# Kernel tuning notes

Hardware: AMD Instinct MI355X
Metric: run time of the kernel (lower is better)

Reference implementation:

```python
import jax, jax.numpy as jnp
import numpy as np

D = 1024
HS = 64
NH = D // HS
NEG_INF = -1e30


def setup_inputs() -> dict:
    key = jax.random.key(0)
    ks = jax.random.split(key, 8)
    B, S = 4, 2048
    x = jax.random.normal(ks[0], (B, S, D), dtype=jnp.float32)
    y = jax.random.normal(ks[1], (B, S, D), dtype=jnp.float32)
    pad_mask = jnp.ones((B, S), dtype=jnp.int32)
    time_attention = jnp.ones((S, S), dtype=jnp.int32)
    scale = 1.0 / np.sqrt(D)
    Wq = jax.random.normal(ks[2], (D, D), dtype=jnp.float32) * scale
    Wk = jax.random.normal(ks[3], (D, D), dtype=jnp.float32) * scale
    Wv = jax.random.normal(ks[4], (D, D), dtype=jnp.float32) * scale
    Wp = jax.random.normal(ks[5], (D, D), dtype=jnp.float32) * scale
    bp = jnp.zeros((D,), dtype=jnp.float32)
    return {"x": x, "y": y, "pad_mask": pad_mask, "time_attention": time_attention,
            "Wq": Wq, "Wk": Wk, "Wv": Wv, "Wp": Wp, "bp": bp}


def reference(x, y, pad_mask, time_attention, Wq, Wk, Wv, Wp, bp):
    B, S, _ = x.shape
    Sy = y.shape[1]
    # q/k/v projections (Linear: x @ W.T), split into heads -> [B, H, S, hs]
    q = (y @ Wq.T).reshape(B, Sy, NH, HS).transpose(0, 2, 1, 3)
    k = (x @ Wk.T).reshape(B, S, NH, HS).transpose(0, 2, 1, 3)
    v = (x @ Wv.T).reshape(B, S, NH, HS).transpose(0, 2, 1, 3)
    # scaled scores [B, H, Sy, S]
    att = jnp.einsum('bhqe,bhke->bhqk', q, k) * (HS ** -0.5)
    # causal mask (tril[:S, :S])
    causal = jnp.tril(jnp.ones((S, S), dtype=jnp.bool_))
    att = jnp.where(causal[None, None, :Sy, :], att, NEG_INF)
    # pad mask over kv positions
    att = jnp.where(pad_mask[:, None, None, :] != 0, att, NEG_INF)
    # time attention mask [Sq, Sk]
    att = jnp.where(time_attention[None, None, :Sy, :] != 0, att, NEG_INF)
    p = jax.nn.softmax(att, axis=-1)  # dropout p=0 -> identity
    out = jnp.einsum('bhqk,bhke->bhqe', p, v)
    out = out.transpose(0, 2, 1, 3).reshape(B, Sy, D)
    return out @ Wp.T + bp
```

## Files before the change

### kernel.cpp

```cpp
#include <hip/hip_runtime.h>
#include <hip/hip_bf16.h>
#include <stdint.h>
#include <stddef.h>


typedef __attribute__((ext_vector_type(4))) float f32x4;
typedef __attribute__((ext_vector_type(8))) short s16x8;
typedef __attribute__((ext_vector_type(4))) float float4v;
typedef __attribute__((ext_vector_type(4))) int i32x4;
typedef __attribute__((ext_vector_type(2))) unsigned int u32x2;

#define DEV __device__ __forceinline__

constexpr int Bsz = 4, Sseq = 2048, Dm = 1024, NHn = 16, HSn = 64;
constexpr float QSCALE = 0.125f * 1.4426950408889634f;

constexpr size_t SZ_BF_XY = (size_t)Bsz * Sseq * Dm * 2;
constexpr size_t SZ_W     = (size_t)Dm * Dm * 2;
constexpr size_t OFF_XBF  = 0;
constexpr size_t OFF_YBF  = OFF_XBF + SZ_BF_XY;
constexpr size_t OFF_WQ   = OFF_YBF + SZ_BF_XY;
constexpr size_t OFF_WK   = OFF_WQ + SZ_W;
constexpr size_t OFF_WV   = OFF_WK + SZ_W;
constexpr size_t OFF_WP   = OFF_WV + SZ_W;
constexpr size_t OFF_QWS  = OFF_WP + SZ_W;
constexpr size_t OFF_KWS  = OFF_QWS + SZ_BF_XY;
constexpr size_t OFF_VTWS = OFF_KWS + SZ_BF_XY;
constexpr size_t OFF_OWS  = OFF_VTWS + SZ_BF_XY;
constexpr size_t OFF_FLAG = OFF_OWS + SZ_BF_XY;

DEV unsigned short f2bf(float f) {
  union { float f; unsigned int u; } v; v.f = f;
  unsigned int r = (v.u + 0x7FFFu + ((v.u >> 16) & 1u)) >> 16;
  return (unsigned short)r;
}

DEV void gll16(const void* g, void* l) {
  __builtin_amdgcn_global_load_lds((const __attribute__((address_space(1))) unsigned int*)g,
                                   (__attribute__((address_space(3))) unsigned int*)l, 16, 0, 0);
}

DEV unsigned int cvtpk(float a, float b) {
  unsigned int r;
  asm("v_cvt_pk_bf16_f32 %0, %1, %2" : "=v"(r) : "v"(a), "v"(b));
  return r;
}

__global__ void cvt_all(const float* __restrict__ x, const float* __restrict__ y,
                        const float* __restrict__ Wq, const float* __restrict__ Wk,
                        const float* __restrict__ Wv, const float* __restrict__ Wp,
                        const int* __restrict__ pad, const int* __restrict__ tmask,
                        char* __restrict__ ws, int* __restrict__ flags) {
  const int blk = blockIdx.x;
  if (blk >= 10240) {
    int bad = 0;
    if (blk < 10248) {
      const i32x4 v = ((const i32x4*)pad)[(blk - 10240) * 256 + threadIdx.x];
      bad = (v[0] == 0) | (v[1] == 0) | (v[2] == 0) | (v[3] == 0);
    } else {
      const i32x4* tp = (const i32x4*)tmask + ((size_t)(blk - 10248) * 256 + threadIdx.x) * 2;
      i32x4 v0 = tp[0], v1 = tp[1];
      bad = (v0[0] == 0) | (v0[1] == 0) | (v0[2] == 0) | (v0[3] == 0) |
            (v1[0] == 0) | (v1[1] == 0) | (v1[2] == 0) | (v1[3] == 0);
    }
    if (__builtin_amdgcn_ballot_w64(bad) != 0 && (threadIdx.x & 63) == 0)
      atomicOr(flags, 1);
    return;
  }
  const float* src;
  unsigned short* dst;
  int b8;
  float scale = 1.f;
  if (blk < 4096)      { src = x;  dst = (unsigned short*)(ws + OFF_XBF); b8 = blk; }
  else if (blk < 8192) { src = y;  dst = (unsigned short*)(ws + OFF_YBF); b8 = blk - 4096; }
  else if (blk < 8704) { src = Wq; dst = (unsigned short*)(ws + OFF_WQ);  b8 = blk - 8192; scale = QSCALE; }
  else if (blk < 9216) { src = Wk; dst = (unsigned short*)(ws + OFF_WK);  b8 = blk - 8704; }
  else if (blk < 9728) { src = Wv; dst = (unsigned short*)(ws + OFF_WV);  b8 = blk - 9216; }
  else                 { src = Wp; dst = (unsigned short*)(ws + OFF_WP);  b8 = blk - 9728; }
  const size_t i = (size_t)b8 * 256 + threadIdx.x;
  const float4v* s = (const float4v*)src + i * 2;
  float4v a = s[0], b = s[1];
  s16x8 o;
  o[0] = (short)f2bf(a[0] * scale); o[1] = (short)f2bf(a[1] * scale);
  o[2] = (short)f2bf(a[2] * scale); o[3] = (short)f2bf(a[3] * scale);
  o[4] = (short)f2bf(b[0] * scale); o[5] = (short)f2bf(b[1] * scale);
  o[6] = (short)f2bf(b[2] * scale); o[7] = (short)f2bf(b[3] * scale);
  *(s16x8*)(dst + i * 8) = o;
}

__global__ __launch_bounds__(256) void q_gemm(const unsigned short* __restrict__ A,
                                              const unsigned short* __restrict__ W,
                                              unsigned short* __restrict__ outb) {
  constexpr int K = 1024;
  __shared__ unsigned short sm[8192];
  unsigned short* lA = sm;
  unsigned short* lB = sm + 4096;
  const int tid = threadIdx.x;
  const int w = tid >> 6, lane = tid & 63, lo = lane & 15, hi = lane >> 4;
  const int wm = w >> 1, wn = w & 1;
  const int m0 = blockIdx.x * 128, n0 = blockIdx.y * 128;
  f32x4 acc[4][4] = {};

  for (int k0 = 0; k0 < K; k0 += 32) {
#pragma unroll
    for (int h = 0; h < 2; ++h) {
      int c = w * 64 + h * 256 + lane;
      gll16(A + (size_t)(m0 + (c >> 2)) * K + k0 + (c & 3) * 8, lA + (size_t)(w * 64 + h * 256) * 8);
      gll16(W + (size_t)(n0 + (c >> 2)) * K + k0 + (c & 3) * 8, lB + (size_t)(w * 64 + h * 256) * 8);
    }
    __syncthreads();
    s16x8 af[4], bfr[4];
#pragma unroll
    for (int mi = 0; mi < 4; ++mi) af[mi] = *(const s16x8*)&lA[(wm * 64 + mi * 16 + lo) * 32 + hi * 8];
#pragma unroll
    for (int ni = 0; ni < 4; ++ni) bfr[ni] = *(const s16x8*)&lB[(wn * 64 + ni * 16 + lo) * 32 + hi * 8];
#pragma unroll
    for (int mi = 0; mi < 4; ++mi)
#pragma unroll
      for (int ni = 0; ni < 4; ++ni)
        acc[mi][ni] = __builtin_amdgcn_mfma_f32_16x16x32_bf16(af[mi], bfr[ni], acc[mi][ni], 0, 0, 0);
    __syncthreads();
  }
#pragma unroll
  for (int mi = 0; mi < 4; ++mi)
#pragma unroll
    for (int ni = 0; ni < 4; ++ni)
#pragma unroll
      for (int j = 0; j < 4; ++j) {
        int m = m0 + wm * 64 + mi * 16 + hi * 4 + j;
        int n = n0 + wn * 64 + ni * 16 + lo;
        int b = m >> 11, s = m & 2047, hh = n >> 6, e = n & 63;
        outb[((size_t)(b * NHn + hh) * Sseq + s) * HSn + e] = f2bf(acc[mi][ni][j]);
      }
}

__global__ __launch_bounds__(256, 2) void kv_gemm(const unsigned short* __restrict__ A,
                                                  const unsigned short* __restrict__ Wk,
                                                  const unsigned short* __restrict__ Wv,
                                                  unsigned short* __restrict__ kws,
                                                  unsigned short* __restrict__ vtw) {
  constexpr int K = 1024;
  __shared__ unsigned short sm[17408];
  unsigned short* lA = sm;
  unsigned short* lBk = sm + 4096;
  unsigned short* lBv = sm + 8192;
  const int tid = threadIdx.x;
  const int w = tid >> 6, lane = tid & 63, lo = lane & 15, hi = lane >> 4;
  const int wm = w >> 1, wn = w & 1;
  const int m0 = blockIdx.x * 128, n0 = blockIdx.y * 128;
  f32x4 acck[4][4] = {}, accv[4][4] = {};

  for (int k0 = 0; k0 < K; k0 += 32) {
#pragma unroll
    for (int h = 0; h < 2; ++h) {
      int c = w * 64 + h * 256 + lane;
      size_t roff = (size_t)(c >> 2) * K + k0 + (c & 3) * 8;
      size_t loff = (size_t)(w * 64 + h * 256) * 8;
      gll16(A + (size_t)m0 * K + roff, lA + loff);
      gll16(Wk + (size_t)n0 * K + roff, lBk + loff);
      gll16(Wv + (size_t)n0 * K + roff, lBv + loff);
    }
    __syncthreads();
    s16x8 af[4], bfk[4], bfv[4];
#pragma unroll
    for (int mi = 0; mi < 4; ++mi) af[mi] = *(const s16x8*)&lA[(wm * 64 + mi * 16 + lo) * 32 + hi * 8];
#pragma unroll
    for (int ni = 0; ni < 4; ++ni) {
      bfk[ni] = *(const s16x8*)&lBk[(wn * 64 + ni * 16 + lo) * 32 + hi * 8];
      bfv[ni] = *(const s16x8*)&lBv[(wn * 64 + ni * 16 + lo) * 32 + hi * 8];
    }
#pragma unroll
    for (int mi = 0; mi < 4; ++mi)
#pragma unroll
      for (int ni = 0; ni < 4; ++ni) {
        acck[mi][ni] = __builtin_amdgcn_mfma_f32_16x16x32_bf16(af[mi], bfk[ni], acck[mi][ni], 0, 0, 0);
        accv[mi][ni] = __builtin_amdgcn_mfma_f32_16x16x32_bf16(af[mi], bfv[ni], accv[mi][ni], 0, 0, 0);
      }
    __syncthreads();
  }

#pragma unroll
  for (int mi = 0; mi < 4; ++mi)
#pragma unroll
    for (int ni = 0; ni < 4; ++ni)
#pragma unroll
      for (int j = 0; j < 4; ++j) {
        int m = m0 + wm * 64 + mi * 16 + hi * 4 + j;
        int n = n0 + wn * 64 + ni * 16 + lo;
        int b = m >> 11, s = m & 2047, hh = n >> 6, e = n & 63;
        kws[((size_t)(b * NHn + hh) * Sseq + s) * HSn + e] = f2bf(acck[mi][ni][j]);
      }
  __syncthreads();
#pragma unroll
  for (int mi = 0; mi < 4; ++mi)
#pragma unroll
    for (int ni = 0; ni < 4; ++ni)
#pragma unroll
      for (int j = 0; j < 4; ++j) {
        int ml = wm * 64 + mi * 16 + hi * 4 + j;
        int nl = wn * 64 + ni * 16 + lo;
        sm[(size_t)nl * 136 + ml] = f2bf(accv[mi][ni][j]);
      }
  __syncthreads();
  int nl = tid >> 1, half = tid & 1;
  int b = m0 >> 11, hh = (n0 + nl) >> 6, e = (n0 + nl) & 63;
  unsigned short* dst = vtw + ((size_t)(b * NHn + hh) * HSn + e) * Sseq + (m0 & 2047) + half * 64;
#pragma unroll
  for (int i = 0; i < 8; ++i)
    *(s16x8*)(dst + i * 8) = *(const s16x8*)&sm[(size_t)nl * 136 + half * 64 + i * 8];
}

__global__ __launch_bounds__(256) void gemm_p(const unsigned short* __restrict__ A,
                                              const unsigned short* __restrict__ W,
                                              float* __restrict__ outf,
                                              const float* __restrict__ bias) {
  constexpr int K = 1024;
  __shared__ unsigned short sm[8192];
  unsigned short* lA = sm;
  unsigned short* lB = sm + 4096;
  const int tid = threadIdx.x;
  const int w = tid >> 6, lane = tid & 63, lo = lane & 15, hi = lane >> 4;
  const int wm = w >> 1, wn = w & 1;
  const int m0 = blockIdx.x * 128, n0 = blockIdx.y * 128;
  f32x4 acc[4][4] = {};
  for (int k0 = 0; k0 < K; k0 += 32) {
#pragma unroll
    for (int h = 0; h < 2; ++h) {
      int c = w * 64 + h * 256 + lane;
      gll16(A + (size_t)(m0 + (c >> 2)) * K + k0 + (c & 3) * 8, lA + (size_t)(w * 64 + h * 256) * 8);
      gll16(W + (size_t)(n0 + (c >> 2)) * K + k0 + (c & 3) * 8, lB + (size_t)(w * 64 + h * 256) * 8);
    }
    __syncthreads();
    s16x8 af[4], bfr[4];
#pragma unroll
    for (int mi = 0; mi < 4; ++mi) af[mi] = *(const s16x8*)&lA[(wm * 64 + mi * 16 + lo) * 32 + hi * 8];
#pragma unroll
    for (int ni = 0; ni < 4; ++ni) bfr[ni] = *(const s16x8*)&lB[(wn * 64 + ni * 16 + lo) * 32 + hi * 8];
#pragma unroll
    for (int mi = 0; mi < 4; ++mi)
#pragma unroll
      for (int ni = 0; ni < 4; ++ni)
        acc[mi][ni] = __builtin_amdgcn_mfma_f32_16x16x32_bf16(af[mi], bfr[ni], acc[mi][ni], 0, 0, 0);
    __syncthreads();
  }
  float bv[4];
#pragma unroll
  for (int ni = 0; ni < 4; ++ni) bv[ni] = bias[n0 + wn * 64 + ni * 16 + lo];
#pragma unroll
  for (int mi = 0; mi < 4; ++mi)
#pragma unroll
    for (int ni = 0; ni < 4; ++ni)
#pragma unroll
      for (int j = 0; j < 4; ++j) {
        int m = m0 + wm * 64 + mi * 16 + hi * 4 + j;
        int n = n0 + wn * 64 + ni * 16 + lo;
        outf[(size_t)m * 1024 + n] = acc[mi][ni][j] + bv[ni];
      }
}

DEV void attn_unit16(const unsigned short* __restrict__ kbc,
                     const unsigned short* __restrict__ vbc,
                     const s16x8 (&qf)[2], f32x4 (&oacc)[4],
                     float& mrun, float& lrun,
                     unsigned short* __restrict__ pbw,
                     int k0, int qw0, int lo, int hi, int b,
                     const int* __restrict__ pad, const int* __restrict__ tmask,
                     bool trivial) {
  if (k0 > qw0 + 15) return;

  f32x4 st[4];
#pragma unroll
  for (int t = 0; t < 4; ++t) {
    f32x4 z = {0.f, 0.f, 0.f, 0.f};
#pragma unroll
    for (int kk = 0; kk < 2; ++kk) {
      s16x8 kfr = *(const s16x8*)&kbc[(t * 16 + lo) * 72 + kk * 32 + hi * 8];
      z = __builtin_amdgcn_mfma_f32_16x16x32_bf16(kfr, qf[kk], z, 0, 0, 0);
    }
    st[t] = z;
  }
  const int qg = qw0 + lo;
  if (k0 + 63 > qw0) {
#pragma unroll
    for (int t = 0; t < 4; ++t)
#pragma unroll
      for (int j = 0; j < 4; ++j)
        if (k0 + t * 16 + hi * 4 + j > qg) st[t][j] = -3e38f;
  }
  if (!trivial) {
#pragma unroll
    for (int t = 0; t < 4; ++t)
#pragma unroll
      for (int j = 0; j < 4; ++j) {
        int kg = k0 + t * 16 + hi * 4 + j;
        if (!pad[b * Sseq + kg] || !tmask[(size_t)qg * Sseq + kg]) st[t][j] = -3e38f;
      }
  }
  float m0v = fmaxf(fmaxf(st[0][0], st[0][1]), fmaxf(st[0][2], st[0][3]));
  float m1v = fmaxf(fmaxf(st[1][0], st[1][1]), fmaxf(st[1][2], st[1][3]));
  float m2v = fmaxf(fmaxf(st[2][0], st[2][1]), fmaxf(st[2][2], st[2][3]));
  float m3v = fmaxf(fmaxf(st[3][0], st[3][1]), fmaxf(st[3][2], st[3][3]));
  float mx = fmaxf(fmaxf(m0v, m1v), fmaxf(m2v, m3v));
  mx = fmaxf(mx, __shfl_xor(mx, 16, 64));
  mx = fmaxf(mx, __shfl_xor(mx, 32, 64));
  const float mnew = fmaxf(mrun, mx);
  const float al = __builtin_amdgcn_exp2f(mrun - mnew);
  mrun = mnew;
  float r0 = 0.f, r1 = 0.f, r2 = 0.f, r3 = 0.f;
#pragma unroll
  for (int j = 0; j < 4; ++j) {
    float p0 = __builtin_amdgcn_exp2f(st[0][j] - mnew); st[0][j] = p0; r0 += p0;
    float p1 = __builtin_amdgcn_exp2f(st[1][j] - mnew); st[1][j] = p1; r1 += p1;
    float p2 = __builtin_amdgcn_exp2f(st[2][j] - mnew); st[2][j] = p2; r2 += p2;
    float p3 = __builtin_amdgcn_exp2f(st[3][j] - mnew); st[3][j] = p3; r3 += p3;
  }
  float rs = (r0 + r1) + (r2 + r3);
  rs += __shfl_xor(rs, 16, 64);
  rs += __shfl_xor(rs, 32, 64);
  lrun = lrun * al + rs;
#pragma unroll
  for (int et = 0; et < 4; ++et) oacc[et] *= al;
#pragma unroll
  for (int t = 0; t < 4; ++t) {
    u32x2 dd = {cvtpk(st[t][0], st[t][1]), cvtpk(st[t][2], st[t][3])};
    *(u32x2*)&pbw[lo * 72 + t * 16 + hi * 4] = dd;
  }
  s16x8 pf[2];
#pragma unroll
  for (int kk = 0; kk < 2; ++kk)
    pf[kk] = *(const s16x8*)&pbw[lo * 72 + kk * 32 + hi * 8];
#pragma unroll
  for (int et = 0; et < 4; ++et)
#pragma unroll
    for (int kk = 0; kk < 2; ++kk) {
      s16x8 vfr = *(const s16x8*)&vbc[(et * 16 + lo) * 72 + kk * 32 + hi * 8];
      oacc[et] = __builtin_amdgcn_mfma_f32_16x16x32_bf16(vfr, pf[kk], oacc[et], 0, 0, 0);
    }
}

DEV void attn_epi16(f32x4 (&oacc)[4], float lrun,
                    unsigned short* __restrict__ pbw,
                    unsigned short* __restrict__ O, int b, int hh, int qw0,
                    int lane, int lo, int hi) {
  const float inv = 1.f / lrun;
#pragma unroll
  for (int et = 0; et < 4; ++et) {
    f32x4 o = oacc[et] * inv;
    u32x2 d = {cvtpk(o[0], o[1]), cvtpk(o[2], o[3])};
    *(u32x2*)&pbw[lo * 72 + et * 16 + hi * 4] = d;
  }
  int q = lane >> 2, seg = lane & 3;
  unsigned short* dst = O + ((size_t)b * Sseq + qw0 + q) * Dm + hh * HSn + seg * 16;
  *(s16x8*)dst = *(const s16x8*)&pbw[q * 72 + seg * 16];
  *(s16x8*)(dst + 8) = *(const s16x8*)&pbw[q * 72 + seg * 16 + 8];
}

__global__ __launch_bounds__(512, 4) void attn_kernel(const unsigned short* __restrict__ Q,
                                                      const unsigned short* __restrict__ Kg,
                                                      const unsigned short* __restrict__ Vt,
                                                      unsigned short* __restrict__ O,
                                                      const int* __restrict__ pad,
                                                      const int* __restrict__ tmask,
                                                      const int* __restrict__ flags) {
  __shared__ unsigned short kb[2][64 * 72];
  __shared__ unsigned short vb[2][64 * 72];
  __shared__ unsigned short pb[8][16 * 72];

  const int ip = blockIdx.x, bh = blockIdx.y;
  const int b = bh >> 4, hh = bh & 15;
  const int tid = threadIdx.x, w = tid >> 6, lane = tid & 63, lo = lane & 15, hi = lane >> 4;
  const int qtA = ip, qtB = 15 - ip;
  const int qw0A = qtA * 128 + w * 16, qw0B = qtB * 128 + w * 16;
  const int ktA = 2 * qtA + 1;
  const int ktmax = 2 * qtB + 2;
  const bool trivial = flags[0] == 0;

  const unsigned short* Qb = Q + (size_t)bh * Sseq * HSn;
  const unsigned short* Kb = Kg + (size_t)bh * Sseq * HSn;
  const unsigned short* Vb = Vt + (size_t)bh * HSn * Sseq;

  s16x8 qfA[2], qfB[2];
#pragma unroll
  for (int kk = 0; kk < 2; ++kk) {
    qfA[kk] = *(const s16x8*)&Qb[(size_t)(qw0A + lo) * HSn + kk * 32 + hi * 8];
    qfB[kk] = *(const s16x8*)&Qb[(size_t)(qw0B + lo) * HSn + kk * 32 + hi * 8];
  }

  f32x4 oaccA[4] = {}, oaccB[4] = {};
  float mrunA = -3e38f, lrunA = 0.f, mrunB = -3e38f, lrunB = 0.f;

  const int shalf = tid >> 8, st_t = tid & 255;
  const int sr = st_t >> 2, sc = (st_t & 3) * 16;

  s16x8 r0, r1;
  if (shalf == 0) {
    const unsigned short* gk = Kb + (size_t)sr * HSn + sc;
    r0 = *(const s16x8*)gk; r1 = *(const s16x8*)(gk + 8);
    *(s16x8*)&kb[0][sr * 72 + sc] = r0; *(s16x8*)&kb[0][sr * 72 + sc + 8] = r1;
  } else {
    const unsigned short* gv = Vb + (size_t)sr * Sseq + sc;
    r0 = *(const s16x8*)gv; r1 = *(const s16x8*)(gv + 8);
    *(s16x8*)&vb[0][sr * 72 + sc] = r0; *(s16x8*)&vb[0][sr * 72 + sc + 8] = r1;
  }
  __syncthreads();

  for (int kt = 0; kt < ktmax; ++kt) {
    const int cur = kt & 1, k0 = kt * 64;
    const bool pre = (kt + 1 < ktmax);
    if (pre) {
      const int k1 = k0 + 64;
      if (shalf == 0) {
        const unsigned short* gk = Kb + (size_t)(k1 + sr) * HSn + sc;
        r0 = *(const s16x8*)gk; r1 = *(const s16x8*)(gk + 8);
      } else {
        const unsigned short* gv = Vb + (size_t)sr * Sseq + k1 + sc;
        r0 = *(const s16x8*)gv; r1 = *(const s16x8*)(gv + 8);
      }
    }
    const unsigned short* kbc = kb[cur];
    const unsigned short* vbc = vb[cur];
    if (kt <= ktA)
      attn_unit16(kbc, vbc, qfA, oaccA, mrunA, lrunA, pb[w],
                  k0, qw0A, lo, hi, b, pad, tmask, trivial);
    attn_unit16(kbc, vbc, qfB, oaccB, mrunB, lrunB, pb[w],
                k0, qw0B, lo, hi, b, pad, tmask, trivial);
    if (pre) {
      const int nb = cur ^ 1;
      if (shalf == 0) {
        *(s16x8*)&kb[nb][sr * 72 + sc] = r0; *(s16x8*)&kb[nb][sr * 72 + sc + 8] = r1;
      } else {
        *(s16x8*)&vb[nb][sr * 72 + sc] = r0; *(s16x8*)&vb[nb][sr * 72 + sc + 8] = r1;
      }
    }
    __syncthreads();
  }

  attn_epi16(oaccA, lrunA, pb[w], O, b, hh, qw0A, lane, lo, hi);
  attn_epi16(oaccB, lrunB, pb[w], O, b, hh, qw0B, lane, lo, hi);
}

extern "C" void kernel_launch(void* const* d_in, const int* in_sizes, int n_in,
                              void* d_out, int out_size, void* d_ws, size_t ws_size,
                              hipStream_t stream) {
  const float* x = (const float*)d_in[0];
  const float* y = (const float*)d_in[1];
  const int* pad = (const int*)d_in[2];
  const int* tmask = (const int*)d_in[3];
  const float* Wq = (const float*)d_in[4];
  const float* Wk = (const float*)d_in[5];
  const float* Wv = (const float*)d_in[6];
  const float* Wp = (const float*)d_in[7];
  const float* bp = (const float*)d_in[8];

  char* ws = (char*)d_ws;
  unsigned short* xbf = (unsigned short*)(ws + OFF_XBF);
  unsigned short* ybf = (unsigned short*)(ws + OFF_YBF);
  unsigned short* wqb = (unsigned short*)(ws + OFF_WQ);
  unsigned short* wkb = (unsigned short*)(ws + OFF_WK);
  unsigned short* wvb = (unsigned short*)(ws + OFF_WV);
  unsigned short* wpb = (unsigned short*)(ws + OFF_WP);
  unsigned short* qws = (unsigned short*)(ws + OFF_QWS);
  unsigned short* kws = (unsigned short*)(ws + OFF_KWS);
  unsigned short* vtw = (unsigned short*)(ws + OFF_VTWS);
  unsigned short* ows = (unsigned short*)(ws + OFF_OWS);
  int* flags = (int*)(ws + OFF_FLAG);

  hipMemsetAsync(flags, 0, 4, stream);
  cvt_all<<<12296, 256, 0, stream>>>(x, y, Wq, Wk, Wv, Wp, pad, tmask, ws, flags);

  q_gemm<<<dim3(64, 8), 256, 0, stream>>>(ybf, wqb, qws);
  kv_gemm<<<dim3(64, 8), 256, 0, stream>>>(xbf, wkb, wvb, kws, vtw);

  attn_kernel<<<dim3(8, 64), 512, 0, stream>>>(qws, kws, vtw, ows, pad, tmask, flags);

  gemm_p<<<dim3(64, 8), 256, 0, stream>>>(ows, wpb, (float*)d_out, bp);
}
```

Before: 199.6 us.

## Skip softmax rescale below threshold and compute row sums via MFMA

Adds a lazy-rescale rule to the online softmax: the running max and the accumulator rescale are updated only when some lane's new max exceeds the old one by more than a threshold, checked wave-uniformly with __all. The row-sum shuffle reduction is replaced by MFMA calls that multiply the bf16 probabilities by a vector of ones, accumulating the denominator in a matrix register. This removes exp/shuffle/scalar work from the VALU path but adds two MFMAs per tile. The denominator is now summed from bf16-rounded probabilities, which matches what the PV product uses.

```diff
diff --git a/kernel.cpp b/kernel.cpp
--- a/kernel.cpp
+++ b/kernel.cpp
@@ -260,8 +260,8 @@
 
 DEV void attn_unit16(const unsigned short* __restrict__ kbc,
                      const unsigned short* __restrict__ vbc,
-                     const s16x8 (&qf)[2], f32x4 (&oacc)[4],
-                     float& mrun, float& lrun,
+                     const s16x8 (&qf)[2], f32x4 (&oacc)[4], f32x4& lacc,
+                     float& mrun, const s16x8& ones,
                      unsigned short* __restrict__ pbw,
                      int k0, int qw0, int lo, int hi, int b,
                      const int* __restrict__ pad, const int* __restrict__ tmask,
@@ -303,23 +303,19 @@
   float mx = fmaxf(fmaxf(m0v, m1v), fmaxf(m2v, m3v));
   mx = fmaxf(mx, __shfl_xor(mx, 16, 64));
   mx = fmaxf(mx, __shfl_xor(mx, 32, 64));
-  const float mnew = fmaxf(mrun, mx);
-  const float al = __builtin_amdgcn_exp2f(mrun - mnew);
-  mrun = mnew;
-  float r0 = 0.f, r1 = 0.f, r2 = 0.f, r3 = 0.f;
-#pragma unroll
-  for (int j = 0; j < 4; ++j) {
-    float p0 = __builtin_amdgcn_exp2f(st[0][j] - mnew); st[0][j] = p0; r0 += p0;
-    float p1 = __builtin_amdgcn_exp2f(st[1][j] - mnew); st[1][j] = p1; r1 += p1;
-    float p2 = __builtin_amdgcn_exp2f(st[2][j] - mnew); st[2][j] = p2; r2 += p2;
-    float p3 = __builtin_amdgcn_exp2f(st[3][j] - mnew); st[3][j] = p3; r3 += p3;
-  }
-  float rs = (r0 + r1) + (r2 + r3);
-  rs += __shfl_xor(rs, 16, 64);
-  rs += __shfl_xor(rs, 32, 64);
-  lrun = lrun * al + rs;
-#pragma unroll
-  for (int et = 0; et < 4; ++et) oacc[et] *= al;
+  if (!__all(mx <= mrun + 11.f)) {
+    const float mnew = fmaxf(mrun, mx);
+    const float al = __builtin_amdgcn_exp2f(mrun - mnew);
+    mrun = mnew;
+#pragma unroll
+    for (int et = 0; et < 4; ++et) oacc[et] *= al;
+    lacc *= al;
+  }
+#pragma unroll
+  for (int t = 0; t < 4; ++t)
+#pragma unroll
+    for (int j = 0; j < 4; ++j)
+      st[t][j] = __builtin_amdgcn_exp2f(st[t][j] - mrun);
 #pragma unroll
   for (int t = 0; t < 4; ++t) {
     u32x2 dd = {cvtpk(st[t][0], st[t][1]), cvtpk(st[t][2], st[t][3])};
@@ -336,6 +332,8 @@
       s16x8 vfr = *(const s16x8*)&vbc[(et * 16 + lo) * 72 + kk * 32 + hi * 8];
       oacc[et] = __builtin_amdgcn_mfma_f32_16x16x32_bf16(vfr, pf[kk], oacc[et], 0, 0, 0);
     }
+  lacc = __builtin_amdgcn_mfma_f32_16x16x32_bf16(ones, pf[0], lacc, 0, 0, 0);
+  lacc = __builtin_amdgcn_mfma_f32_16x16x32_bf16(ones, pf[1], lacc, 0, 0, 0);
 }
 
 DEV void attn_epi16(f32x4 (&oacc)[4], float lrun,
@@ -386,8 +384,13 @@
     qfB[kk] = *(const s16x8*)&Qb[(size_t)(qw0B + lo) * HSn + kk * 32 + hi * 8];
   }
 
+  s16x8 ones;
+#pragma unroll
+  for (int j = 0; j < 8; ++j) ones[j] = (short)0x3F80;
+
   f32x4 oaccA[4] = {}, oaccB[4] = {};
-  float mrunA = -3e38f, lrunA = 0.f, mrunB = -3e38f, lrunB = 0.f;
+  f32x4 laccA = {}, laccB = {};
+  float mrunA = -3e38f, mrunB = -3e38f;
 
   const int shalf = tid >> 8, st_t = tid & 255;
   const int sr = st_t >> 2, sc = (st_t & 3) * 16;
@@ -420,9 +423,9 @@
     const unsigned short* kbc = kb[cur];
     const unsigned short* vbc = vb[cur];
     if (kt <= ktA)
-      attn_unit16(kbc, vbc, qfA, oaccA, mrunA, lrunA, pb[w],
+      attn_unit16(kbc, vbc, qfA, oaccA, laccA, mrunA, ones, pb[w],
                   k0, qw0A, lo, hi, b, pad, tmask, trivial);
-    attn_unit16(kbc, vbc, qfB, oaccB, mrunB, lrunB, pb[w],
+    attn_unit16(kbc, vbc, qfB, oaccB, laccB, mrunB, ones, pb[w],
                 k0, qw0B, lo, hi, b, pad, tmask, trivial);
     if (pre) {
       const int nb = cur ^ 1;
@@ -435,8 +438,8 @@
     __syncthreads();
   }
 
-  attn_epi16(oaccA, lrunA, pb[w], O, b, hh, qw0A, lane, lo, hi);
-  attn_epi16(oaccB, lrunB, pb[w], O, b, hh, qw0B, lane, lo, hi);
+  attn_epi16(oaccA, laccA[0], pb[w], O, b, hh, qw0A, lane, lo, hi);
+  attn_epi16(oaccB, laccB[0], pb[w], O, b, hh, qw0B, lane, lo, hi);
 }
 
 extern "C" void kernel_launch(void* const* d_in, const int* in_sizes, int n_in,
```

New measurement: 192.8 us. -3.4%, faster.
